# Optimization experiments

Hardware: AMD Instinct MI355X
Metric: run time of the kernel (lower is better)

Reference implementation:

```python
import jax, jax.numpy as jnp
import numpy as np

V, D, H, L, FF, NA, NB, S, C, BS = 32000, 768, 12, 6, 3072, 2, 2, 512, 10, 16
MOE_LAYERS = (1, 3, 5)
NE = NA * NB


def _ln(x, g, b, eps=1e-5):
    m = x.mean(-1, keepdims=True)
    v = ((x - m) ** 2).mean(-1, keepdims=True)
    return (x - m) / jnp.sqrt(v + eps) * g + b


def _ffn(x, W1, B1, W2, B2):
    # GLU-style FFN: w2(a * silu(b)) where [a, b] = chunk(w1(x), 2)
    h = x @ W1.T + B1
    a, b = jnp.split(h, 2, -1)
    return (a * jax.nn.silu(b)) @ W2.T + B2


def _mha(x, wqkv, bqkv, wo, bo):
    Bq, Sq, d = x.shape
    dh = d // H
    qkv = x @ wqkv.T + bqkv
    q, k, v = jnp.split(qkv, 3, -1)
    q = q.reshape(Bq, Sq, H, dh).transpose(0, 2, 1, 3)
    k = k.reshape(Bq, Sq, H, dh).transpose(0, 2, 1, 3)
    v = v.reshape(Bq, Sq, H, dh).transpose(0, 2, 1, 3)
    scores = jnp.einsum('bhqd,bhkd->bhqk', q, k) / jnp.sqrt(jnp.float32(dh))
    attn = jax.nn.softmax(scores, axis=-1)
    o = jnp.einsum('bhqk,bhkd->bhqd', attn, v)
    o = o.transpose(0, 2, 1, 3).reshape(Bq, Sq, d)
    return o @ wo.T + bo


def _moe(xf, W1, B1, W2, B2, gAw, gAb, gBw, gBb):
    pA = jax.nn.softmax(xf @ gAw.T + gAb, axis=-1)  # [T, NA]
    pB = jax.nn.softmax(xf @ gBw.T + gBb, axis=-1)  # [T, NB]
    iA = jnp.argmax(pA, -1)
    iB = jnp.argmax(pB, -1)
    auxA = NA * (pA.mean(0) * jax.nn.one_hot(iA, NA).mean(0)).sum()
    auxB = NB * (pB.mean(0) * jax.nn.one_hot(iB, NB).mean(0)).sum()
    e = iA * NB + iB  # [T] flattened expert id
    # dense all-expert compute then per-token select (E is small = 4)
    h = jnp.einsum('td,efd->etf', xf, W1) + B1[:, None, :]  # [NE, T, 2*FF]
    a, b = jnp.split(h, 2, -1)
    y = jnp.einsum('etf,edf->etd', a * jax.nn.silu(b), W2) + B2[:, None, :]
    out = y[e, jnp.arange(xf.shape[0])]  # [T, D]
    return out, auxA + auxB


def _forward(tok_emb, pos_emb, wqkv, bqkv, wo, bo, ln1g, ln1b, ln2g, ln2b,
             dW1, dB1, dW2, dB2, mW1, mB1, mW2, mB2, gAw, gAb, gBw, gBb,
             cW1, cB1, cW2, cB2, input_ids):
    x = tok_emb[input_ids] + pos_emb[None, :, :]
    total_aux = jnp.float32(0.0)
    di = mi = 0
    for l in range(L):
        x = _ln(x + _mha(x, wqkv[l], bqkv[l], wo[l], bo[l]), ln1g[l], ln1b[l])
        if l in MOE_LAYERS:
            xf = x.reshape(BS * S, D)
            f, aux = _moe(xf, mW1[mi], mB1[mi], mW2[mi], mB2[mi],
                          gAw[mi], gAb[mi], gBw[mi], gBb[mi])
            mi += 1
            total_aux = total_aux + aux
            f = f.reshape(BS, S, D)
        else:
            f = _ffn(x, dW1[di], dB1[di], dW2[di], dB2[di])
            di += 1
        x = _ln(x + f, ln2g[l], ln2b[l])
    rep = x.mean(1)  # mean pooling (no cls token / mask)
    hcls = jax.nn.relu(rep @ cW1.T + cB1)
    logits = hcls @ cW2.T + cB2
    return logits, total_aux


def setup_inputs() -> dict:
    key = jax.random.key(0)
    ks = iter(jax.random.split(key, 48))
    r = lambda shape, s=0.02: jax.random.normal(next(ks), shape, jnp.float32) * s
    Ld, Lm = L - len(MOE_LAYERS), len(MOE_LAYERS)
    return dict(
        input_ids=jax.random.randint(next(ks), (BS, S), 0, V),
        tok_emb=r((V, D)),
        pos_emb=r((S, D), 0.01),
        wqkv=r((L, 3 * D, D)), bqkv=jnp.zeros((L, 3 * D), jnp.float32),
        wo=r((L, D, D)), bo=jnp.zeros((L, D), jnp.float32),
        ln1g=jnp.ones((L, D), jnp.float32), ln1b=jnp.zeros((L, D), jnp.float32),
        ln2g=jnp.ones((L, D), jnp.float32), ln2b=jnp.zeros((L, D), jnp.float32),
        dW1=r((Ld, 2 * FF, D)), dB1=jnp.zeros((Ld, 2 * FF), jnp.float32),
        dW2=r((Ld, D, FF)), dB2=jnp.zeros((Ld, D), jnp.float32),
        mW1=r((Lm, NE, 2 * FF, D)), mB1=jnp.zeros((Lm, NE, 2 * FF), jnp.float32),
        mW2=r((Lm, NE, D, FF)), mB2=jnp.zeros((Lm, NE, D), jnp.float32),
        gAw=r((Lm, NA, D)), gAb=jnp.zeros((Lm, NA), jnp.float32),
        gBw=r((Lm, NB, D)), gBb=jnp.zeros((Lm, NB), jnp.float32),
        cW1=r((D, D)), cB1=jnp.zeros((D,), jnp.float32),
        cW2=r((C, D)), cB2=jnp.zeros((C,), jnp.float32),
    )


def reference(input_ids, tok_emb, pos_emb, wqkv, bqkv, wo, bo, ln1g, ln1b,
              ln2g, ln2b, dW1, dB1, dW2, dB2, mW1, mB1, mW2, mB2,
              gAw, gAb, gBw, gBb, cW1, cB1, cW2, cB2):
    return _forward(tok_emb, pos_emb, wqkv, bqkv, wo, bo, ln1g, ln1b, ln2g,
                    ln2b, dW1, dB1, dW2, dB2, mW1, mB1, mW2, mB2,
                    gAw, gAb, gBw, gBb, cW1, cB1, cW2, cB2, input_ids)
```

## Files before the change

kernel.cpp:

```cpp
#include <hip/hip_runtime.h>
#include <cstddef>

#define TOK   8192
#define DIMD  768
#define NH    12
#define DHD   64
#define SEQ   512
#define NB_   16
#define FFD   3072
#define NEXP  4
#define CCLS  10
#define FF2   (2*FFD)

typedef short bf16x8 __attribute__((ext_vector_type(8)));
typedef float f32x4  __attribute__((ext_vector_type(4)));

static const size_t OFF_X    = 0;
static const size_t OFF_XB   = OFF_X   + (size_t)TOK*DIMD;
static const size_t OFF_F    = OFF_XB  + (size_t)TOK*DIMD/2;
static const size_t OFF_SH   = OFF_F   + (size_t)TOK*DIMD;
static const size_t SH_FL    = (size_t)8704*FF2/2;
static const size_t OFF_WQ   = OFF_SH  + SH_FL;
static const size_t OFF_WOB  = OFF_WQ  + (size_t)3*DIMD*DIMD/2;
static const size_t OFF_W1B  = OFF_WOB + (size_t)DIMD*DIMD/2;
static const size_t OFF_W2B  = OFF_W1B + (size_t)NEXP*FF2*DIMD/2;
static const size_t OFF_REP  = OFF_W2B + (size_t)NEXP*DIMD*FFD/2;
static const size_t OFF_HCLS = OFF_REP + (size_t)NB_*DIMD;
static const size_t OFF_STAT = OFF_HCLS+ (size_t)NB_*DIMD;
static const size_t OFF_INT  = OFF_STAT+ 8;
static const size_t OFF_AUX  = OFF_INT + 160;
static const size_t OFF_EID  = OFF_AUX + 1;
static const size_t OFF_PERM = OFF_EID + TOK;

__device__ __forceinline__ ushort f2bf(float f) {
    union { float f; unsigned u; } v; v.f = f;
    unsigned r = v.u + 0x7FFF + ((v.u >> 16) & 1);
    return (ushort)(r >> 16);
}
__device__ __forceinline__ float bf2f(ushort u) {
    union { unsigned u; float f; } v; v.u = ((unsigned)u) << 16;
    return v.f;
}
__device__ __forceinline__ void gload16(const void* g, void* l) {
    __builtin_amdgcn_global_load_lds((const __attribute__((address_space(1))) void*)g,
                                     (__attribute__((address_space(3))) void*)l, 16, 0, 0);
}

__global__ __launch_bounds__(256) void k_cvt(const float* __restrict__ s, ushort* __restrict__ d, int n8)
{
    int i = blockIdx.x * 256 + threadIdx.x;
    if (i >= n8) return;
    float4 x0 = ((const float4*)s)[i * 2];
    float4 x1 = ((const float4*)s)[i * 2 + 1];
    ushort r[8] = { f2bf(x0.x), f2bf(x0.y), f2bf(x0.z), f2bf(x0.w),
                    f2bf(x1.x), f2bf(x1.y), f2bf(x1.z), f2bf(x1.w) };
    ((uint4*)d)[i] = *(uint4*)r;
}

__global__ __launch_bounds__(256) void k_embed(const int* __restrict__ ids,
                                               const float* __restrict__ te,
                                               const float* __restrict__ pe,
                                               float* __restrict__ x,
                                               ushort* __restrict__ xb)
{
    int i = blockIdx.x * 256 + threadIdx.x;
    const int nd4 = DIMD / 4;
    if (i >= TOK * nd4) return;
    int t = i / nd4, d4 = i % nd4;
    int s = t % SEQ;
    int id = ids[t];
    float4 a = ((const float4*)(te + (size_t)id * DIMD))[d4];
    float4 b = ((const float4*)(pe + (size_t)s  * DIMD))[d4];
    float4 o; o.x = a.x + b.x; o.y = a.y + b.y; o.z = a.z + b.z; o.w = a.w + b.w;
    ((float4*)(x + (size_t)t * DIMD))[d4] = o;
    ushort4 ob = make_ushort4(f2bf(o.x), f2bf(o.y), f2bf(o.z), f2bf(o.w));
    *(ushort4*)(xb + (size_t)t * DIMD + d4 * 4) = ob;
}

__global__ __launch_bounds__(256) void k_gluip(ushort* __restrict__ h)
{
    int i = blockIdx.x * 256 + threadIdx.x;
    const int nf8 = FFD / 8;
    int row = i / nf8, j8 = i % nf8;
    size_t base = (size_t)row * FF2 + j8 * 8;
    uint4 a8 = *(const uint4*)(h + base);
    uint4 b8 = *(const uint4*)(h + base + FFD);
    const ushort* ap = (const ushort*)&a8;
    const ushort* bp = (const ushort*)&b8;
    ushort r[8];
#pragma unroll
    for (int j = 0; j < 8; ++j) {
        float a = bf2f(ap[j]), b = bf2f(bp[j]);
        r[j] = f2bf(a * (b / (1.f + __expf(-b))));
    }
    *(uint4*)(h + base) = *(uint4*)r;
}

template<int GATHER, int CBF, int SCAT>
__global__ __launch_bounds__(256) void k_mm(const ushort* __restrict__ A,
                                            const ushort* __restrict__ Wb,
                                            const float* __restrict__ bias,
                                            void* __restrict__ C_,
                                            int N, int K, int lda,
                                            const int* __restrict__ perm,
                                            const int* __restrict__ offs,
                                            const int* __restrict__ blke,
                                            const int* __restrict__ blkb,
                                            const int* __restrict__ nblk)
{
    constexpr int MOE = GATHER || SCAT;
    __shared__ ushort As[2][4096];
    __shared__ ushort Bs[2][4096];
    __shared__ int    toks[128];
    const int tid = threadIdx.x, lane = tid & 63, w = tid >> 6;
    {
    }
    int bid = blockIdx.y * gridDim.x + blockIdx.x;
    int nwg = gridDim.x * gridDim.y;
    int q = nwg >> 3, r8 = nwg & 7;
    int xcd = bid & 7, loc = bid >> 3;
    int lbid = (xcd < r8 ? xcd * (q + 1) : r8 * (q + 1) + (xcd - r8) * q) + loc;
    const int bx = lbid % gridDim.x, by = lbid / gridDim.x;
    const int n0 = bx * 128, row0 = by * 128;
    const ushort* W = Wb;
    const float*  bi = bias;
    int lb = 0, cnt = 1 << 30;
    if constexpr (MOE) {
        if (by >= *nblk) return;
        int e = blke[by];
        lb = blkb[by];
        int base = offs[e];
        cnt = offs[e + 1] - base;
        W  += (size_t)e * N * K;
        bi += (size_t)e * N;
        if (tid < 128) { int rg = lb + tid; toks[tid] = perm[base + (rg < cnt ? rg : cnt - 1)]; }
        __syncthreads();
    }
    int ar0, ar1;
    if constexpr (GATHER) { ar0 = toks[lane]; ar1 = toks[64 + lane]; }
    else                  { ar0 = row0 + lane; ar1 = row0 + 64 + lane; }
    const ushort* ap0 = A + (size_t)ar0 * lda + w * 8;
    const ushort* ap1 = A + (size_t)ar1 * lda + w * 8;
    const ushort* bp0 = W + (size_t)(n0 + lane) * K + w * 8;
    const ushort* bp1 = W + (size_t)(n0 + 64 + lane) * K + w * 8;

    const int l15 = lane & 15, l4 = lane >> 4;
    const int wm = w >> 1, wn = w & 1;
    f32x4 acc[4][4] = {};

    gload16(ap0, &As[0][w * 1024]);
    gload16(ap1, &As[0][w * 1024 + 512]);
    gload16(bp0, &Bs[0][w * 1024]);
    gload16(bp1, &Bs[0][w * 1024 + 512]);
    __syncthreads();

    const int NT = K / 32;
    int cur = 0;
    for (int t = 0; t < NT; ++t) {
        if (t + 1 < NT) {
            int ko = (t + 1) * 32;
            gload16(ap0 + ko, &As[cur ^ 1][w * 1024]);
            gload16(ap1 + ko, &As[cur ^ 1][w * 1024 + 512]);
            gload16(bp0 + ko, &Bs[cur ^ 1][w * 1024]);
            gload16(bp1 + ko, &Bs[cur ^ 1][w * 1024 + 512]);
        }
        bf16x8 af[4], bf_[4];
#pragma unroll
        for (int i = 0; i < 4; ++i) {
            af[i]  = *(const bf16x8*)&As[cur][l4 * 1024 + (wm * 64 + i * 16 + l15) * 8];
            bf_[i] = *(const bf16x8*)&Bs[cur][l4 * 1024 + (wn * 64 + i * 16 + l15) * 8];
        }
#pragma unroll
        for (int mi = 0; mi < 4; ++mi)
#pragma unroll
            for (int ni = 0; ni < 4; ++ni)
                acc[mi][ni] = __builtin_amdgcn_mfma_f32_16x16x32_bf16(af[mi], bf_[ni], acc[mi][ni], 0, 0, 0);
        __syncthreads();
        cur ^= 1;
    }
#pragma unroll
    for (int ni = 0; ni < 4; ++ni) {
        int col = n0 + wn * 64 + ni * 16 + l15;
        float bb = bi[col];
#pragma unroll
        for (int mi = 0; mi < 4; ++mi) {
            int ri = wm * 64 + mi * 16 + l4 * 4;
#pragma unroll
            for (int r = 0; r < 4; ++r) {
                float o = acc[mi][ni][r] + bb;
                if constexpr (SCAT) {
                    if (lb + ri + r < cnt)
                        ((float*)C_)[(size_t)toks[ri + r] * N + col] = o;
                } else if constexpr (CBF) {
                    ((ushort*)C_)[(size_t)(row0 + ri + r) * N + col] = f2bf(o);
                } else {
                    ((float*)C_)[(size_t)(row0 + ri + r) * N + col] = o;
                }
            }
        }
    }
}

__global__ __launch_bounds__(256) void k_attn(const ushort* __restrict__ qkv, ushort* __restrict__ out)
{
    __shared__ ushort Qs[64][72];
    __shared__ ushort Ks[64][72];
    __shared__ ushort Vt[64][72];
    __shared__ ushort Ps[4][16][72];
    const int bh = blockIdx.x;
    const int b = bh / NH, h = bh % NH;
    const int qt = blockIdx.y;
    const int tid = threadIdx.x, lane = tid & 63, w = tid >> 6;
    const int l15 = lane & 15, l4 = lane >> 4;
    const int t0 = b * SEQ + qt * 64;
    {
        int r = tid >> 3, c8 = (tid & 7) * 8;
#pragma unroll
        for (int p = 0; p < 2; ++p) {
            int rr = r + p * 32;
            *(uint4*)&Qs[rr][c8] = *(const uint4*)(qkv + (size_t)(t0 + rr) * 3 * DIMD + h * DHD + c8);
        }
    }
    __syncthreads();
    bf16x8 aq[2];
    aq[0] = *(const bf16x8*)&Qs[w*16 + l15][l4*8];
    aq[1] = *(const bf16x8*)&Qs[w*16 + l15][32 + l4*8];
    f32x4 o[4] = {};
    float m[4], lsum[4];
#pragma unroll
    for (int r = 0; r < 4; ++r) { m[r] = -3.0e38f; lsum[r] = 0.f; }
    for (int kt = 0; kt < SEQ; kt += 64) {
        __syncthreads();
        {
            int r = tid >> 3, c8 = (tid & 7) * 8;
#pragma unroll
            for (int p = 0; p < 2; ++p) {
                int rr = r + p * 32;
                const ushort* kp = qkv + (size_t)(b * SEQ + kt + rr) * 3 * DIMD + DIMD + h * DHD;
                *(uint4*)&Ks[rr][c8] = *(const uint4*)(kp + c8);
                uint4 vv = *(const uint4*)(kp + DIMD + c8);
                const ushort* vs = (const ushort*)&vv;
#pragma unroll
                for (int j = 0; j < 8; ++j) Vt[c8 + j][rr] = vs[j];
            }
        }
        __syncthreads();
        f32x4 s[4] = {};
#pragma unroll
        for (int kk = 0; kk < 2; ++kk)
#pragma unroll
            for (int ni = 0; ni < 4; ++ni) {
                bf16x8 bk = *(const bf16x8*)&Ks[ni*16 + l15][kk*32 + l4*8];
                s[ni] = __builtin_amdgcn_mfma_f32_16x16x32_bf16(aq[kk], bk, s[ni], 0, 0, 0);
            }
        float csc[4];
#pragma unroll
        for (int r = 0; r < 4; ++r) {
            float mx = -3.0e38f;
#pragma unroll
            for (int ni = 0; ni < 4; ++ni) { s[ni][r] *= 0.125f; mx = fmaxf(mx, s[ni][r]); }
            mx = fmaxf(mx, __shfl_xor(mx, 1));
            mx = fmaxf(mx, __shfl_xor(mx, 2));
            mx = fmaxf(mx, __shfl_xor(mx, 4));
            mx = fmaxf(mx, __shfl_xor(mx, 8));
            float nm = fmaxf(m[r], mx);
            float c = __expf(m[r] - nm);
            m[r] = nm;
            float ps = 0.f;
#pragma unroll
            for (int ni = 0; ni < 4; ++ni) { s[ni][r] = __expf(s[ni][r] - nm); ps += s[ni][r]; }
            ps += __shfl_xor(ps, 1);
            ps += __shfl_xor(ps, 2);
            ps += __shfl_xor(ps, 4);
            ps += __shfl_xor(ps, 8);
            lsum[r] = lsum[r] * c + ps;
            csc[r] = c;
#pragma unroll
            for (int ni = 0; ni < 4; ++ni)
                Ps[w][l4*4 + r][ni*16 + l15] = f2bf(s[ni][r]);
        }
#pragma unroll
        for (int di = 0; di < 4; ++di)
#pragma unroll
            for (int r = 0; r < 4; ++r) o[di][r] *= csc[r];
        bf16x8 ap[2];
        ap[0] = *(const bf16x8*)&Ps[w][l15][l4*8];
        ap[1] = *(const bf16x8*)&Ps[w][l15][32 + l4*8];
#pragma unroll
        for (int kk = 0; kk < 2; ++kk)
#pragma unroll
            for (int di = 0; di < 4; ++di) {
                bf16x8 bv = *(const bf16x8*)&Vt[di*16 + l15][kk*32 + l4*8];
                o[di] = __builtin_amdgcn_mfma_f32_16x16x32_bf16(ap[kk], bv, o[di], 0, 0, 0);
            }
    }
    float inv[4];
#pragma unroll
    for (int r = 0; r < 4; ++r) inv[r] = 1.f / lsum[r];
#pragma unroll
    for (int di = 0; di < 4; ++di)
#pragma unroll
        for (int r = 0; r < 4; ++r)
            out[(size_t)(t0 + w*16 + l4*4 + r) * DIMD + h * DHD + di*16 + l15] = f2bf(o[di][r] * inv[r]);
}

__global__ __launch_bounds__(256) void k_ln(float* __restrict__ x, const float* __restrict__ f,
                                            const float* __restrict__ g, const float* __restrict__ b,
                                            ushort* __restrict__ xb)
{
    const int t = blockIdx.x, tid = threadIdx.x;
    __shared__ float y[DIMD];
    __shared__ float red[256];
    float* xr = x + (size_t)t * DIMD;
    const float* fr = f + (size_t)t * DIMD;
    float s = 0.f;
    for (int d = tid; d < DIMD; d += 256) { float v = xr[d] + fr[d]; y[d] = v; s += v; }
    red[tid] = s; __syncthreads();
    for (int off = 128; off > 0; off >>= 1) { if (tid < off) red[tid] += red[tid + off]; __syncthreads(); }
    const float mean = red[0] * (1.f / DIMD);
    __syncthreads();
    s = 0.f;
    for (int d = tid; d < DIMD; d += 256) { float v = y[d] - mean; s += v * v; }
    red[tid] = s; __syncthreads();
    for (int off = 128; off > 0; off >>= 1) { if (tid < off) red[tid] += red[tid + off]; __syncthreads(); }
    const float rstd = 1.f / sqrtf(red[0] * (1.f / DIMD) + 1e-5f);
    for (int d = tid; d < DIMD; d += 256) {
        float v = (y[d] - mean) * rstd * g[d] + b[d];
        xr[d] = v;
        xb[(size_t)t * DIMD + d] = f2bf(v);
    }
}

__global__ __launch_bounds__(256) void k_gate(const float* __restrict__ x,
                                              const float* __restrict__ gAw, const float* __restrict__ gAb,
                                              const float* __restrict__ gBw, const float* __restrict__ gBb,
                                              float* __restrict__ sums, int* __restrict__ cnts,
                                              int* __restrict__ e_id)
{
    const int tid = threadIdx.x, lane = tid & 63, wid = tid >> 6;
    const int gw = blockIdx.x * 4 + wid;
    float wA0[12], wA1[12], wB0[12], wB1[12];
#pragma unroll
    for (int i = 0; i < 12; ++i) {
        int d = lane + i * 64;
        wA0[i] = gAw[d]; wA1[i] = gAw[DIMD + d];
        wB0[i] = gBw[d]; wB1[i] = gBw[DIMD + d];
    }
    const float bA0 = gAb[0], bA1 = gAb[1], bB0 = gBb[0], bB1 = gBb[1];
    float sA0 = 0.f, sA1 = 0.f, sB0 = 0.f, sB1 = 0.f;
    int cA1 = 0, cB1 = 0, cE0 = 0, cE1 = 0, cE2 = 0;
    for (int i = 0; i < 32; ++i) {
        int t = gw * 32 + i;
        const float* xr = x + (size_t)t * DIMD;
        float a0 = 0.f, a1 = 0.f, b0 = 0.f, b1 = 0.f;
#pragma unroll
        for (int j = 0; j < 12; ++j) {
            float v = xr[lane + j * 64];
            a0 = fmaf(v, wA0[j], a0); a1 = fmaf(v, wA1[j], a1);
            b0 = fmaf(v, wB0[j], b0); b1 = fmaf(v, wB1[j], b1);
        }
#pragma unroll
        for (int off = 1; off < 64; off <<= 1) {
            a0 += __shfl_xor(a0, off); a1 += __shfl_xor(a1, off);
            b0 += __shfl_xor(b0, off); b1 += __shfl_xor(b1, off);
        }
        a0 += bA0; a1 += bA1; b0 += bB0; b1 += bB1;
        int iA = (a1 > a0) ? 1 : 0;
        int iB = (b1 > b0) ? 1 : 0;
        float mA = fmaxf(a0, a1); float eA0 = __expf(a0 - mA), eA1 = __expf(a1 - mA);
        float dA = 1.f / (eA0 + eA1);
        float mB = fmaxf(b0, b1); float eB0 = __expf(b0 - mB), eB1 = __expf(b1 - mB);
        float dB = 1.f / (eB0 + eB1);
        sA0 += eA0 * dA; sA1 += eA1 * dA;
        sB0 += eB0 * dB; sB1 += eB1 * dB;
        cA1 += iA; cB1 += iB;
        int e = iA * 2 + iB;
        cE0 += (e == 0); cE1 += (e == 1); cE2 += (e == 2);
        if (lane == 0) e_id[t] = e;
    }
    __shared__ float fpart[4][4];
    __shared__ int   ipart[4][8];
    if (lane == 0) {
        fpart[wid][0] = sA0; fpart[wid][1] = sA1; fpart[wid][2] = sB0; fpart[wid][3] = sB1;
        ipart[wid][0] = 32 - cA1; ipart[wid][1] = cA1;
        ipart[wid][2] = 32 - cB1; ipart[wid][3] = cB1;
        ipart[wid][4] = cE0; ipart[wid][5] = cE1; ipart[wid][6] = cE2;
        ipart[wid][7] = 32 - cE0 - cE1 - cE2;
    }
    __syncthreads();
    if (tid < 4)  atomicAdd(sums + tid, fpart[0][tid] + fpart[1][tid] + fpart[2][tid] + fpart[3][tid]);
    else if (tid >= 64 && tid < 72) {
        int k = tid - 64;
        atomicAdd(cnts + k, ipart[0][k] + ipart[1][k] + ipart[2][k] + ipart[3][k]);
    }
}

__global__ void k_offsets(const int* __restrict__ cntE, int* __restrict__ offs, int* __restrict__ cursor,
                          int* __restrict__ nblk, int* __restrict__ blke, int* __restrict__ blkb)
{
    if (threadIdx.x == 0) {
        int a = 0, nb = 0;
        for (int e = 0; e < NEXP; ++e) {
            offs[e] = a; a += cntE[e]; cursor[e] = 0;
            int blocks = (cntE[e] + 127) >> 7;
            for (int b = 0; b < blocks; ++b) { blke[nb] = e; blkb[nb] = b * 128; ++nb; }
        }
        offs[NEXP] = a;
        *nblk = nb;
    }
}

__global__ __launch_bounds__(256) void k_scatter(const int* __restrict__ e_id, const int* __restrict__ offs,
                                                 int* __restrict__ cursor, int* __restrict__ perm)
{
    int t = blockIdx.x * 256 + threadIdx.x;
    int lane = threadIdx.x & 63;
    int e = e_id[t];
#pragma unroll
    for (int eo = 0; eo < NEXP; ++eo) {
        unsigned long long m = __ballot(e == eo);
        if (m == 0ULL) continue;
        int leader = __ffsll((long long)m) - 1;
        int base = 0;
        if (lane == leader) base = atomicAdd(cursor + eo, (int)__popcll(m));
        base = __shfl(base, leader);
        if (e == eo) {
            int lower = (int)__popcll(m & ((1ULL << lane) - 1ULL));
            perm[offs[eo] + base + lower] = t;
        }
    }
}

__global__ void k_aux(const float* __restrict__ sums, const int* __restrict__ cnts, float* __restrict__ aux_acc)
{
    if (threadIdx.x == 0) {
        const float invT2 = 1.f / ((float)TOK * (float)TOK);
        float aA = 2.f * (sums[0] * (float)cnts[0] + sums[1] * (float)cnts[1]) * invT2;
        float aB = 2.f * (sums[2] * (float)cnts[2] + sums[3] * (float)cnts[3]) * invT2;
        *aux_acc += aA + aB;
    }
}

__global__ __launch_bounds__(256) void k_rep(const float* __restrict__ x, float* __restrict__ rep)
{
    int i = blockIdx.x * 256 + threadIdx.x;
    if (i >= NB_ * DIMD) return;
    int b = i / DIMD, d = i % DIMD;
    float s = 0.f;
    for (int q = 0; q < SEQ; ++q) s += x[((size_t)b * SEQ + q) * DIMD + d];
    rep[i] = s * (1.f / SEQ);
}

__global__ __launch_bounds__(256) void k_cls1(const float* __restrict__ rep, const float* __restrict__ cW1,
                                              const float* __restrict__ cB1, float* __restrict__ hcls)
{
    int w = blockIdx.x * 4 + (threadIdx.x >> 6);
    int lane = threadIdx.x & 63;
    if (w >= NB_ * DIMD) return;
    int b = w / DIMD, i = w % DIMD;
    float s = 0.f;
    for (int d = lane; d < DIMD; d += 64) s += rep[b * DIMD + d] * cW1[(size_t)i * DIMD + d];
    for (int off = 32; off > 0; off >>= 1) s += __shfl_down(s, off);
    if (lane == 0) hcls[w] = fmaxf(s + cB1[i], 0.f);
}

__global__ __launch_bounds__(256) void k_cls2(const float* __restrict__ hcls, const float* __restrict__ cW2,
                                              const float* __restrict__ cB2, float* __restrict__ out)
{
    int w = blockIdx.x * 4 + (threadIdx.x >> 6);
    int lane = threadIdx.x & 63;
    if (w >= NB_ * CCLS) return;
    int b = w / CCLS, c = w % CCLS;
    float s = 0.f;
    for (int d = lane; d < DIMD; d += 64) s += hcls[b * DIMD + d] * cW2[(size_t)c * DIMD + d];
    for (int off = 32; off > 0; off >>= 1) s += __shfl_down(s, off);
    if (lane == 0) out[w] = s + cB2[c];
}

__global__ void k_writeaux(const float* __restrict__ aux_acc, float* __restrict__ out)
{
    if (threadIdx.x == 0) out[NB_ * CCLS] = *aux_acc;
}

extern "C" void kernel_launch(void* const* d_in, const int* in_sizes, int n_in,
                              void* d_out, int out_size, void* d_ws, size_t ws_size,
                              hipStream_t stream)
{
    const int*   input_ids = (const int*)  d_in[0];
    const float* tok_emb   = (const float*)d_in[1];
    const float* pos_emb   = (const float*)d_in[2];
    const float* wqkv      = (const float*)d_in[3];
    const float* bqkv      = (const float*)d_in[4];
    const float* wo        = (const float*)d_in[5];
    const float* bo        = (const float*)d_in[6];
    const float* ln1g      = (const float*)d_in[7];
    const float* ln1b      = (const float*)d_in[8];
    const float* ln2g      = (const float*)d_in[9];
    const float* ln2b      = (const float*)d_in[10];
    const float* dW1       = (const float*)d_in[11];
    const float* dB1       = (const float*)d_in[12];
    const float* dW2       = (const float*)d_in[13];
    const float* dB2       = (const float*)d_in[14];
    const float* mW1       = (const float*)d_in[15];
    const float* mB1       = (const float*)d_in[16];
    const float* mW2       = (const float*)d_in[17];
    const float* mB2       = (const float*)d_in[18];
    const float* gAw       = (const float*)d_in[19];
    const float* gAb       = (const float*)d_in[20];
    const float* gBw       = (const float*)d_in[21];
    const float* gBb       = (const float*)d_in[22];
    const float* cW1       = (const float*)d_in[23];
    const float* cB1       = (const float*)d_in[24];
    const float* cW2       = (const float*)d_in[25];
    const float* cB2       = (const float*)d_in[26];

    float* out = (float*)d_out;
    float* ws  = (float*)d_ws;

    float*  X    = ws + OFF_X;
    ushort* XB   = (ushort*)(ws + OFF_XB);
    float*  F    = ws + OFF_F;
    ushort* QKV  = (ushort*)(ws + OFF_SH);
    ushort* G    = (ushort*)(ws + OFF_SH + (size_t)TOK * 3 * DIMD / 2);
    ushort* Hh   = (ushort*)(ws + OFF_SH);
    ushort* WQB  = (ushort*)(ws + OFF_WQ);
    ushort* WOB  = (ushort*)(ws + OFF_WOB);
    ushort* W1B  = (ushort*)(ws + OFF_W1B);
    ushort* W2B  = (ushort*)(ws + OFF_W2B);
    float*  REP  = ws + OFF_REP;
    float*  HCLS = ws + OFF_HCLS;
    float*  SUMS = ws + OFF_STAT;
    int*    INTB = (int*)(ws + OFF_INT);
    int*    CNTS = INTB;
    int*    OFFS = INTB + 8;
    int*    CURS = INTB + 13;
    int*    NBLK = INTB + 17;
    int*    BLKE = INTB + 18;
    int*    BLKB = INTB + 86;
    float*  AUXP = ws + OFF_AUX;
    int*    EID  = (int*)(ws + OFF_EID);
    int*    PERM = (int*)(ws + OFF_PERM);

    hipMemsetAsync(AUXP, 0, sizeof(float), stream);

    k_embed<<<dim3((TOK * DIMD / 4) / 256), 256, 0, stream>>>(input_ids, tok_emb, pos_emb, X, XB);

    int di = 0, mi = 0;
    for (int l = 0; l < 6; ++l) {
        const int moe = (l == 1 || l == 3 || l == 5);
        {
            int n8 = 3 * DIMD * DIMD / 8;
            k_cvt<<<dim3((n8 + 255) / 256), 256, 0, stream>>>(wqkv + (size_t)l * 3 * DIMD * DIMD, WQB, n8);
            n8 = DIMD * DIMD / 8;
            k_cvt<<<dim3((n8 + 255) / 256), 256, 0, stream>>>(wo + (size_t)l * DIMD * DIMD, WOB, n8);
            if (moe) {
                n8 = NEXP * FF2 * DIMD / 8;
                k_cvt<<<dim3((n8 + 255) / 256), 256, 0, stream>>>(mW1 + (size_t)mi * NEXP * FF2 * DIMD, W1B, n8);
                n8 = NEXP * DIMD * FFD / 8;
                k_cvt<<<dim3((n8 + 255) / 256), 256, 0, stream>>>(mW2 + (size_t)mi * NEXP * DIMD * FFD, W2B, n8);
            } else {
                n8 = FF2 * DIMD / 8;
                k_cvt<<<dim3((n8 + 255) / 256), 256, 0, stream>>>(dW1 + (size_t)di * FF2 * DIMD, W1B, n8);
                n8 = DIMD * FFD / 8;
                k_cvt<<<dim3((n8 + 255) / 256), 256, 0, stream>>>(dW2 + (size_t)di * DIMD * FFD, W2B, n8);
            }
        }
        k_mm<0,1,0><<<dim3(3 * DIMD / 128, TOK / 128), 256, 0, stream>>>(
            XB, WQB, bqkv + (size_t)l * 3 * DIMD, QKV, 3 * DIMD, DIMD, DIMD,
            nullptr, nullptr, nullptr, nullptr, nullptr);
        k_attn<<<dim3(NB_ * NH, SEQ / 64), 256, 0, stream>>>(QKV, G);
        k_mm<0,0,0><<<dim3(DIMD / 128, TOK / 128), 256, 0, stream>>>(
            G, WOB, bo + (size_t)l * DIMD, F, DIMD, DIMD, DIMD,
            nullptr, nullptr, nullptr, nullptr, nullptr);
        k_ln<<<TOK, 256, 0, stream>>>(X, F, ln1g + (size_t)l * DIMD, ln1b + (size_t)l * DIMD, XB);

        if (moe) {
            hipMemsetAsync(SUMS, 0, 64, stream);
            k_gate<<<64, 256, 0, stream>>>(X,
                gAw + (size_t)mi * 2 * DIMD, gAb + (size_t)mi * 2,
                gBw + (size_t)mi * 2 * DIMD, gBb + (size_t)mi * 2,
                SUMS, CNTS, EID);
            k_offsets<<<1, 1, 0, stream>>>(CNTS + 4, OFFS, CURS, NBLK, BLKE, BLKB);
            k_scatter<<<TOK / 256, 256, 0, stream>>>(EID, OFFS, CURS, PERM);
            k_mm<1,1,0><<<dim3(FF2 / 128, 68), 256, 0, stream>>>(
                XB, W1B, mB1 + (size_t)mi * NEXP * FF2, Hh, FF2, DIMD, DIMD,
                PERM, OFFS, BLKE, BLKB, NBLK);
            k_gluip<<<dim3(8704 * (FFD / 8) / 256), 256, 0, stream>>>(Hh);
            k_mm<0,0,1><<<dim3(DIMD / 128, 68), 256, 0, stream>>>(
                Hh, W2B, mB2 + (size_t)mi * NEXP * DIMD, F, DIMD, FFD, FF2,
                PERM, OFFS, BLKE, BLKB, NBLK);
            k_aux<<<1, 1, 0, stream>>>(SUMS, CNTS, AUXP);
            ++mi;
        } else {
            k_mm<0,1,0><<<dim3(FF2 / 128, TOK / 128), 256, 0, stream>>>(
                XB, W1B, dB1 + (size_t)di * FF2, Hh, FF2, DIMD, DIMD,
                nullptr, nullptr, nullptr, nullptr, nullptr);
            k_gluip<<<dim3(8704 * (FFD / 8) / 256), 256, 0, stream>>>(Hh);
            k_mm<0,0,0><<<dim3(DIMD / 128, TOK / 128), 256, 0, stream>>>(
                Hh, W2B, dB2 + (size_t)di * DIMD, F, DIMD, FFD, FF2,
                nullptr, nullptr, nullptr, nullptr, nullptr);
            ++di;
        }
        k_ln<<<TOK, 256, 0, stream>>>(X, F, ln2g + (size_t)l * DIMD, ln2b + (size_t)l * DIMD, XB);
    }

    k_rep<<<dim3((NB_ * DIMD + 255) / 256), 256, 0, stream>>>(X, REP);
    k_cls1<<<dim3(NB_ * DIMD / 4), 256, 0, stream>>>(REP, cW1, cB1, HCLS);
    k_cls2<<<dim3((NB_ * CCLS + 3) / 4), 256, 0, stream>>>(HCLS, cW2, cB2, out);
    k_writeaux<<<1, 1, 0, stream>>>(AUXP, out);
}
```

Before: 3.359 ms.

## Fuse GLU activation into W1 GEMM epilogue with paired a/b tiles

Adds a k_w1g kernel that computes matching 128-column tiles of both GLU halves (a and b) in one block, with two accumulator sets, and applies a*silu(b) in the epilogue. It writes only the FF-wide gated result, so the 2*FF intermediate and the separate k_gluip pass are dropped, and W2 reads from a narrower buffer. The price is twice the accumulators per thread and a larger shared B tile, which raises register and LDS pressure and may lower occupancy.

```diff
diff --git a/kernel.cpp b/kernel.cpp
--- a/kernel.cpp
+++ b/kernel.cpp
@@ -77,25 +77,6 @@
     *(ushort4*)(xb + (size_t)t * DIMD + d4 * 4) = ob;
 }
 
-__global__ __launch_bounds__(256) void k_gluip(ushort* __restrict__ h)
-{
-    int i = blockIdx.x * 256 + threadIdx.x;
-    const int nf8 = FFD / 8;
-    int row = i / nf8, j8 = i % nf8;
-    size_t base = (size_t)row * FF2 + j8 * 8;
-    uint4 a8 = *(const uint4*)(h + base);
-    uint4 b8 = *(const uint4*)(h + base + FFD);
-    const ushort* ap = (const ushort*)&a8;
-    const ushort* bp = (const ushort*)&b8;
-    ushort r[8];
-#pragma unroll
-    for (int j = 0; j < 8; ++j) {
-        float a = bf2f(ap[j]), b = bf2f(bp[j]);
-        r[j] = f2bf(a * (b / (1.f + __expf(-b))));
-    }
-    *(uint4*)(h + base) = *(uint4*)r;
-}
-
 template<int GATHER, int CBF, int SCAT>
 __global__ __launch_bounds__(256) void k_mm(const ushort* __restrict__ A,
                                             const ushort* __restrict__ Wb,
@@ -113,8 +94,6 @@
     __shared__ ushort Bs[2][4096];
     __shared__ int    toks[128];
     const int tid = threadIdx.x, lane = tid & 63, w = tid >> 6;
-    {
-    }
     int bid = blockIdx.y * gridDim.x + blockIdx.x;
     int nwg = gridDim.x * gridDim.y;
     int q = nwg >> 3, r8 = nwg & 7;
@@ -196,6 +175,109 @@
                 } else {
                     ((float*)C_)[(size_t)(row0 + ri + r) * N + col] = o;
                 }
+            }
+        }
+    }
+}
+
+template<int MOE>
+__global__ __launch_bounds__(256) void k_w1g(const ushort* __restrict__ A,
+                                             const ushort* __restrict__ Wb,
+                                             const float* __restrict__ bias,
+                                             ushort* __restrict__ G,
+                                             const int* __restrict__ perm,
+                                             const int* __restrict__ offs,
+                                             const int* __restrict__ blke,
+                                             const int* __restrict__ blkb,
+                                             const int* __restrict__ nblk)
+{
+    __shared__ ushort As[2][4096];
+    __shared__ ushort Bs[2][8192];
+    __shared__ int    toks[128];
+    const int tid = threadIdx.x, lane = tid & 63, w = tid >> 6;
+    int bid = blockIdx.y * gridDim.x + blockIdx.x;
+    int nwg = gridDim.x * gridDim.y;
+    int q = nwg >> 3, r8 = nwg & 7;
+    int xcd = bid & 7, loc = bid >> 3;
+    int lbid = (xcd < r8 ? xcd * (q + 1) : r8 * (q + 1) + (xcd - r8) * q) + loc;
+    const int bx = lbid % gridDim.x, by = lbid / gridDim.x;
+    const int n0 = bx * 128, row0 = by * 128;
+    const ushort* W = Wb;
+    const float*  bi = bias;
+    if constexpr (MOE) {
+        if (by >= *nblk) return;
+        int e = blke[by];
+        W  += (size_t)e * FF2 * DIMD;
+        bi += (size_t)e * FF2;
+        int base = offs[e], cnt = offs[e + 1] - base, lb = blkb[by];
+        if (tid < 128) { int rg = lb + tid; toks[tid] = perm[base + (rg < cnt ? rg : cnt - 1)]; }
+        __syncthreads();
+    }
+    int ar0, ar1;
+    if constexpr (MOE) { ar0 = toks[lane]; ar1 = toks[64 + lane]; }
+    else               { ar0 = row0 + lane; ar1 = row0 + 64 + lane; }
+    const ushort* ap0  = A + (size_t)ar0 * DIMD + w * 8;
+    const ushort* ap1  = A + (size_t)ar1 * DIMD + w * 8;
+    const ushort* bpa0 = W + (size_t)(n0 + lane) * DIMD + w * 8;
+    const ushort* bpa1 = W + (size_t)(n0 + 64 + lane) * DIMD + w * 8;
+    const ushort* bpb0 = W + (size_t)(FFD + n0 + lane) * DIMD + w * 8;
+    const ushort* bpb1 = W + (size_t)(FFD + n0 + 64 + lane) * DIMD + w * 8;
+
+    const int l15 = lane & 15, l4 = lane >> 4;
+    const int wm = w >> 1, wn = w & 1;
+    f32x4 accA[4][4] = {}, accB[4][4] = {};
+
+    gload16(ap0,  &As[0][w * 1024]);
+    gload16(ap1,  &As[0][w * 1024 + 512]);
+    gload16(bpa0, &Bs[0][w * 2048]);
+    gload16(bpa1, &Bs[0][w * 2048 + 512]);
+    gload16(bpb0, &Bs[0][w * 2048 + 1024]);
+    gload16(bpb1, &Bs[0][w * 2048 + 1536]);
+    __syncthreads();
+
+    const int NT = DIMD / 32;
+    int cur = 0;
+    for (int t = 0; t < NT; ++t) {
+        if (t + 1 < NT) {
+            int ko = (t + 1) * 32;
+            gload16(ap0 + ko,  &As[cur ^ 1][w * 1024]);
+            gload16(ap1 + ko,  &As[cur ^ 1][w * 1024 + 512]);
+            gload16(bpa0 + ko, &Bs[cur ^ 1][w * 2048]);
+            gload16(bpa1 + ko, &Bs[cur ^ 1][w * 2048 + 512]);
+            gload16(bpb0 + ko, &Bs[cur ^ 1][w * 2048 + 1024]);
+            gload16(bpb1 + ko, &Bs[cur ^ 1][w * 2048 + 1536]);
+        }
+        bf16x8 af[4], ba[4], bb[4];
+#pragma unroll
+        for (int i = 0; i < 4; ++i) {
+            af[i] = *(const bf16x8*)&As[cur][l4 * 1024 + (wm * 64 + i * 16 + l15) * 8];
+            ba[i] = *(const bf16x8*)&Bs[cur][l4 * 2048 + (wn * 64 + i * 16 + l15) * 8];
+            bb[i] = *(const bf16x8*)&Bs[cur][l4 * 2048 + 1024 + (wn * 64 + i * 16 + l15) * 8];
+        }
+#pragma unroll
+        for (int mi = 0; mi < 4; ++mi)
+#pragma unroll
+            for (int ni = 0; ni < 4; ++ni) {
+                accA[mi][ni] = __builtin_amdgcn_mfma_f32_16x16x32_bf16(af[mi], ba[ni], accA[mi][ni], 0, 0, 0);
+                accB[mi][ni] = __builtin_amdgcn_mfma_f32_16x16x32_bf16(af[mi], bb[ni], accB[mi][ni], 0, 0, 0);
+            }
+        __syncthreads();
+        cur ^= 1;
+    }
+#pragma unroll
+    for (int ni = 0; ni < 4; ++ni) {
+        int col = n0 + wn * 64 + ni * 16 + l15;
+        float fa = bi[col];
+        float fb = bi[FFD + col];
+#pragma unroll
+        for (int mi = 0; mi < 4; ++mi) {
+            int ri = wm * 64 + mi * 16 + l4 * 4;
+#pragma unroll
+            for (int r = 0; r < 4; ++r) {
+                float a = accA[mi][ni][r] + fa;
+                float b = accB[mi][ni][r] + fb;
+                float g = a * (b / (1.f + __expf(-b)));
+                G[(size_t)(row0 + ri + r) * FFD + col] = f2bf(g);
             }
         }
     }
@@ -522,7 +604,7 @@
     float*  F    = ws + OFF_F;
     ushort* QKV  = (ushort*)(ws + OFF_SH);
     ushort* G    = (ushort*)(ws + OFF_SH + (size_t)TOK * 3 * DIMD / 2);
-    ushort* Hh   = (ushort*)(ws + OFF_SH);
+    ushort* Gg   = (ushort*)(ws + OFF_SH);
     ushort* WQB  = (ushort*)(ws + OFF_WQ);
     ushort* WOB  = (ushort*)(ws + OFF_WOB);
     ushort* W1B  = (ushort*)(ws + OFF_W1B);
@@ -582,22 +664,20 @@
                 SUMS, CNTS, EID);
             k_offsets<<<1, 1, 0, stream>>>(CNTS + 4, OFFS, CURS, NBLK, BLKE, BLKB);
             k_scatter<<<TOK / 256, 256, 0, stream>>>(EID, OFFS, CURS, PERM);
-            k_mm<1,1,0><<<dim3(FF2 / 128, 68), 256, 0, stream>>>(
-                XB, W1B, mB1 + (size_t)mi * NEXP * FF2, Hh, FF2, DIMD, DIMD,
+            k_w1g<1><<<dim3(FFD / 128, 68), 256, 0, stream>>>(
+                XB, W1B, mB1 + (size_t)mi * NEXP * FF2, Gg,
                 PERM, OFFS, BLKE, BLKB, NBLK);
-            k_gluip<<<dim3(8704 * (FFD / 8) / 256), 256, 0, stream>>>(Hh);
             k_mm<0,0,1><<<dim3(DIMD / 128, 68), 256, 0, stream>>>(
-                Hh, W2B, mB2 + (size_t)mi * NEXP * DIMD, F, DIMD, FFD, FF2,
+                Gg, W2B, mB2 + (size_t)mi * NEXP * DIMD, F, DIMD, FFD, FFD,
                 PERM, OFFS, BLKE, BLKB, NBLK);
             k_aux<<<1, 1, 0, stream>>>(SUMS, CNTS, AUXP);
             ++mi;
         } else {
-            k_mm<0,1,0><<<dim3(FF2 / 128, TOK / 128), 256, 0, stream>>>(
-                XB, W1B, dB1 + (size_t)di * FF2, Hh, FF2, DIMD, DIMD,
+            k_w1g<0><<<dim3(FFD / 128, TOK / 128), 256, 0, stream>>>(
+                XB, W1B, dB1 + (size_t)di * FF2, Gg,
                 nullptr, nullptr, nullptr, nullptr, nullptr);
-            k_gluip<<<dim3(8704 * (FFD / 8) / 256), 256, 0, stream>>>(Hh);
             k_mm<0,0,0><<<dim3(DIMD / 128, TOK / 128), 256, 0, stream>>>(
-                Hh, W2B, dB2 + (size_t)di * DIMD, F, DIMD, FFD, FF2,
+                Gg, W2B, dB2 + (size_t)di * DIMD, F, DIMD, FFD, FFD,
                 nullptr, nullptr, nullptr, nullptr, nullptr);
             ++di;
         }
```

New measurement: 3.089 ms. 8.0% less time.
